# Kernel tuning notes

Measured on AMD Instinct MI355X. Metric: run time of the kernel, lower is better.

Reference implementation:

```python
import jax, jax.numpy as jnp
import numpy as np
from jax import lax

B = 8            # IMAGES_PER_GPU
A = 261888       # num_anchors (1024x1024 Mask R-CNN FPN anchors)
PRE_NMS_LIMIT = 6000
PROPOSAL_COUNT = 1000
NMS_THRESHOLD = 0.7


def setup_inputs() -> dict:
    key = jax.random.key(0)
    k1, k2, k3, k4 = jax.random.split(key, 4)
    rpn_probs = jax.random.uniform(k1, (B, A, 2), dtype=jnp.float32)
    rpn_bbox = jax.random.normal(k2, (B, A, 4), dtype=jnp.float32)
    # valid normalized anchors: y1,x1 in [0,0.9], height/width in [0.01,0.1]
    yx = jax.random.uniform(k3, (B, A, 2), minval=0.0, maxval=0.9)
    hw = jax.random.uniform(k4, (B, A, 2), minval=0.01, maxval=0.1)
    anchors = jnp.concatenate([yx, yx + hw], axis=-1)  # (y1, x1, y2, x2)
    return {"rpn_probs": rpn_probs, "rpn_bbox": rpn_bbox, "anchors": anchors}


def _apply_box_deltas(boxes, deltas):
    # boxes, deltas: [..., 4] in (y1, x1, y2, x2) / (dy, dx, log(dh), log(dw))
    h = boxes[..., 2] - boxes[..., 0]
    w = boxes[..., 3] - boxes[..., 1]
    cy = boxes[..., 0] + 0.5 * h + deltas[..., 0] * h
    cx = boxes[..., 1] + 0.5 * w + deltas[..., 1] * w
    h = h * jnp.exp(deltas[..., 2])
    w = w * jnp.exp(deltas[..., 3])
    y1 = cy - 0.5 * h
    x1 = cx - 0.5 * w
    return jnp.stack([y1, x1, y1 + h, x1 + w], axis=-1)


def _nms_single(boxes, scores):
    # boxes: [K, 4] already sorted by score descending; greedy NMS, zero-padded
    areas = (boxes[:, 2] - boxes[:, 0]) * (boxes[:, 3] - boxes[:, 1])

    def step(valid, _):
        idx = jnp.argmax(valid)          # first still-valid = highest score
        has = valid[idx]                 # False when no candidates remain
        box = boxes[idx]
        yy1 = jnp.maximum(box[0], boxes[:, 0])
        xx1 = jnp.maximum(box[1], boxes[:, 1])
        yy2 = jnp.minimum(box[2], boxes[:, 2])
        xx2 = jnp.minimum(box[3], boxes[:, 3])
        inter = jnp.maximum(yy2 - yy1, 0.0) * jnp.maximum(xx2 - xx1, 0.0)
        union = (box[2] - box[0]) * (box[3] - box[1]) + areas - inter
        iou = lax.stop_gradient(jnp.where(union > 0, inter / union, 0.0))
        valid = valid & (iou <= NMS_THRESHOLD)  # also suppresses idx (self IoU = 1)
        return valid, jnp.where(has, box, jnp.zeros_like(box))

    _, selected = lax.scan(step, jnp.ones(boxes.shape[0], dtype=bool), None,
                           length=PROPOSAL_COUNT)
    return selected  # [PROPOSAL_COUNT, 4], zero-padded like tf.pad in original


def reference(rpn_probs, rpn_bbox, anchors):
    std = jnp.asarray([0.1, 0.1, 0.2, 0.2], dtype=rpn_bbox.dtype)  # RPN_BBOX_STD_DEV
    scores = rpn_probs[:, :, 1]                 # fg prob [B, A]
    deltas = rpn_bbox * std
    k = min(PRE_NMS_LIMIT, anchors.shape[1])
    top_scores, ix = lax.top_k(scores, k)       # sorted descending, [B, K]
    idx = ix[..., None]
    deltas_k = jnp.take_along_axis(deltas, idx, axis=1)    # [B, K, 4]
    anchors_k = jnp.take_along_axis(anchors, idx, axis=1)  # [B, K, 4]
    boxes = jnp.clip(_apply_box_deltas(anchors_k, deltas_k), 0.0, 1.0)  # window [0,0,1,1]
    return jax.vmap(_nms_single)(boxes, top_scores)  # [B, PROPOSAL_COUNT, 4]
```

## Files before the change

kernel.cpp:

```cpp
#include <hip/hip_runtime.h>
#include <math.h>
#include <stdint.h>

typedef uint32_t u32; typedef uint64_t u64; typedef uint16_t u16; typedef int32_t i32;

#define BATCH 8
#define NA    261888
#define SEGS  32
#define SEGCHUNK 8184
#define WCHUNK 2046
#define SUBCAP 64
#define NSUB  128
#define TOPK  6000
#define PROP  1000
#define TOP1  1024
#define TMPCAP 2048
#define CACHEB 8192
#define FBMAX 16384
#define NW64  16
#define PSTATIC 0x3F7C0000u

#define OFF_FBK   0
#define OFF_CACHE 1048576
#define OFF_CNT   1572864
#define OFF_STAT  1576960
#define OFF_BOX   1577216
#define OFF_AREA  1708288
#define OFF_MASK  1741056
#define WS_NEEDED 2789632


__device__ __forceinline__ void decode_box(const float4 an, const float4 dl,
                                           float4& bx, float& ar) {
    float d0 = __fmul_rn(dl.x, 0.1f), d1 = __fmul_rn(dl.y, 0.1f);
    float d2 = __fmul_rn(dl.z, 0.2f), d3 = __fmul_rn(dl.w, 0.2f);
    float h = __fsub_rn(an.z, an.x), w = __fsub_rn(an.w, an.y);
    float cy = __fadd_rn(__fadd_rn(an.x, __fmul_rn(0.5f, h)), __fmul_rn(d0, h));
    float cx = __fadd_rn(__fadd_rn(an.y, __fmul_rn(0.5f, w)), __fmul_rn(d1, w));
    float h2 = __fmul_rn(h, (float)exp((double)d2));
    float w2 = __fmul_rn(w, (float)exp((double)d3));
    float y1 = __fsub_rn(cy, __fmul_rn(0.5f, h2));
    float x1 = __fsub_rn(cx, __fmul_rn(0.5f, w2));
    float y2 = __fadd_rn(y1, h2);
    float x2 = __fadd_rn(x1, w2);
    y1 = fminf(fmaxf(y1, 0.f), 1.f); x1 = fminf(fmaxf(x1, 0.f), 1.f);
    y2 = fminf(fmaxf(y2, 0.f), 1.f); x2 = fminf(fmaxf(x2, 0.f), 1.f);
    bx = make_float4(y1, x1, y2, x2);
    ar = __fmul_rn(__fsub_rn(y2, y1), __fsub_rn(x2, x1));
}

__device__ __forceinline__ bool sup_pred(const float4 bi, const float ai,
                                         const float4 bj, const float aj) {
    const double tmid = (double)0.7f + 0x1p-25;
    float yy1 = fmaxf(bi.x, bj.x), xx1 = fmaxf(bi.y, bj.y);
    float yy2 = fminf(bi.z, bj.z), xx2 = fminf(bi.w, bj.w);
    float ih = fmaxf(__fsub_rn(yy2, yy1), 0.f);
    float iw = fmaxf(__fsub_rn(xx2, xx1), 0.f);
    float inter = __fmul_rn(ih, iw);
    float uni = __fsub_rn(__fadd_rn(ai, aj), inter);
    return (uni > 0.f) && ((double)inter >= tmid * (double)uni);
}

__global__ __launch_bounds__(256) void k_histcache(const float4* __restrict__ p4,
                                                   u64* __restrict__ cache,
                                                   u32* __restrict__ cnt) {
    const int b = blockIdx.y, seg = blockIdx.x;
    const int wave = threadIdx.x >> 6, lane = threadIdx.x & 63;
    const u64 lmask = (1ull << lane) - 1ull;
    const size_t fbase = ((size_t)b * NA + seg * SEGCHUNK + wave * WCHUNK) >> 1;
    const u32 abase = (u32)(seg * SEGCHUNK + wave * WCHUNK);
    u64* cseg = cache + (size_t)b * CACHEB + (seg * 4 + wave) * SUBCAP;
    u32 wOff = 0;
    #pragma unroll
    for (int it = 0; it < 16; ++it) {
        int f = it * 64 + lane;
        bool ok = f < (WCHUNK / 2);
        u32 bitsA = 0, bitsB = 0;
        if (ok) {
            float4 v = p4[fbase + f];
            bitsA = __float_as_uint(v.y);
            bitsB = __float_as_uint(v.w);
        }
        bool pA = ok && bitsA >= PSTATIC;
        bool pB = ok && bitsB >= PSTATIC;
        u64 mA = __ballot(pA);
        u64 mB = __ballot(pB);
        u32 cA = (u32)__popcll(mA);
        if (pA) {
            u32 slot = wOff + (u32)__popcll(mA & lmask);
            if (slot < SUBCAP) cseg[slot] = ((u64)(~bitsA) << 32) | (u64)(abase + 2 * f);
        }
        if (pB) {
            u32 slot = wOff + cA + (u32)__popcll(mB & lmask);
            if (slot < SUBCAP) cseg[slot] = ((u64)(~bitsB) << 32) | (u64)(abase + 2 * f + 1);
        }
        wOff += cA + (u32)__popcll(mB);
    }
    if (lane == 0) cnt[b * NSUB + seg * 4 + wave] = wOff;
}

__global__ __launch_bounds__(1024) void k_sortdec(const u64* __restrict__ cache,
                                                  const u32* __restrict__ cnt,
                                                  const float4* __restrict__ anchors,
                                                  const float4* __restrict__ bbox,
                                                  u32* __restrict__ stat_g,
                                                  float4* __restrict__ boxes,
                                                  float* __restrict__ areas) {
    __shared__ u32 hist[4096];
    __shared__ u32 suffix[4096];
    __shared__ u32 ps[256];
    __shared__ u32 psS[257];
    __shared__ u64 tmp[TMPCAP];
    __shared__ u32 scnt[NSUB];
    __shared__ u32 wq[4];
    __shared__ u32 sP, sN, sBin, stat;
    const int b = blockIdx.x;
    const int tid = threadIdx.x;
    const int lane = tid & 63, wv = tid >> 6;
    if (tid == 0) { stat = 1u; sBin = 0xFFFFFFFFu; }
    for (int i = tid; i < 4096; i += 1024) hist[i] = 0;
    __syncthreads();
    if (tid < NSUB) {
        u32 raw = cnt[b * NSUB + tid];
        scnt[tid] = raw > SUBCAP ? SUBCAP : raw;
        if (raw > SUBCAP) stat = 0u;
    }
    __syncthreads();
    for (int t = tid; t < CACHEB; t += 1024) {
        int sub = t >> 6, off = t & (SUBCAP - 1);
        if (off < (int)scnt[sub]) {
            u32 bits = ~((u32)(cache[(size_t)b * CACHEB + t] >> 32));
            atomicAdd(&hist[(bits >> 6) & 0xFFFu], 1u);
        }
    }
    __syncthreads();
    if (tid < 256) {
        u32 su = 0;
        #pragma unroll
        for (int k = 0; k < 16; ++k) su += hist[tid * 16 + k];
        ps[tid] = su;
    }
    __syncthreads();
    {
        u32 v = (tid < 256) ? ps[tid] : 0u;
        #pragma unroll
        for (int d = 1; d < 64; d <<= 1) {
            u32 o = __shfl_down(v, d);
            if (lane + d < 64) v += o;
        }
        if (tid < 256 && lane == 0) wq[wv] = v;
        __syncthreads();
        if (tid < 256) {
            u32 add = 0;
            for (int q = wv + 1; q < 4; ++q) add += wq[q];
            psS[tid] = v + add;
        }
        if (tid == 0) psS[256] = 0u;
        __syncthreads();
    }
    {
        const int t4 = tid * 4;
        const int seg = tid >> 2;
        const int segEnd = seg * 16 + 15;
        u32 tail = 0;
        for (int bb = t4 + 4; bb <= segEnd; ++bb) tail += hist[bb];
        u32 h0 = hist[t4], h1 = hist[t4 + 1], h2 = hist[t4 + 2], h3 = hist[t4 + 3];
        u32 s3 = psS[seg + 1] + tail;
        u32 s2 = s3 + h3;
        u32 s1 = s2 + h2;
        u32 s0 = s1 + h1;
        suffix[t4] = s0; suffix[t4 + 1] = s1; suffix[t4 + 2] = s2; suffix[t4 + 3] = s3;
        if (s0 < TOP1 && s0 + h0 >= TOP1) sBin = (u32)t4;
        if (s1 < TOP1 && s1 + h1 >= TOP1) sBin = (u32)(t4 + 1);
        if (s2 < TOP1 && s2 + h2 >= TOP1) sBin = (u32)(t4 + 2);
        if (s3 < TOP1 && s3 + h3 >= TOP1) sBin = (u32)(t4 + 3);
    }
    __syncthreads();
    if (tid == 0) {
        if (sBin == 0xFFFFFFFFu) stat = 0u;
        else {
            sP = PSTATIC + (sBin << 6);
            u32 n = suffix[sBin] + hist[sBin];
            sN = n;
            if (n > TMPCAP) stat = 0u;
        }
    }
    __syncthreads();
    if (stat) {
        for (int i = tid; i < 4096; i += 1024) hist[i] = 0;
        __syncthreads();
        const u32 P = sP;
        for (int t = tid; t < CACHEB; t += 1024) {
            int sub = t >> 6, off = t & (SUBCAP - 1);
            if (off < (int)scnt[sub]) {
                u64 key = cache[(size_t)b * CACHEB + t];
                u32 bits = ~((u32)(key >> 32));
                if (bits >= P) {
                    u32 bin = (bits >> 6) & 0xFFFu;
                    u32 arr = atomicAdd(&hist[bin], 1u);
                    tmp[suffix[bin] + arr] = key;
                }
            }
        }
        __syncthreads();
        const u32 n = sN;
        for (u32 t = (u32)tid; t < n; t += 1024) {
            u64 key = tmp[t];
            u32 bits = ~((u32)(key >> 32));
            u32 bin = (bits >> 6) & 0xFFFu;
            u32 base = suffix[bin], len = hist[bin];
            u32 pos = base;
            for (u32 q = base; q < base + len; ++q) pos += (tmp[q] < key) ? 1u : 0u;
            if (pos < TOP1) {
                u32 idx = (u32)key;
                float4 bx; float ar;
                decode_box(anchors[(size_t)b * NA + idx], bbox[(size_t)b * NA + idx], bx, ar);
                boxes[b * TOP1 + pos] = bx;
                areas[b * TOP1 + pos] = ar;
            }
        }
    }
    if (tid == 0) stat_g[b] = stat;
}

__global__ __launch_bounds__(256) void k_mask(const float4* __restrict__ boxes,
                                              const float* __restrict__ areas,
                                              u32* __restrict__ mw32) {
    const int b = blockIdx.y;
    const int wave = threadIdx.x >> 6, lane = threadIdx.x & 63;
    const int irow = blockIdx.x * 4 + wave;
    const int cmax = irow >> 6;
    u32* mt = mw32 + (size_t)b * (NW64 * TOP1 * 2);
    float4 bi = boxes[b * TOP1 + irow];
    float  ai = areas[b * TOP1 + irow];
    u32 myw = 0;
    for (int c = 0; c <= cmax; ++c) {
        float4 bj = boxes[b * TOP1 + c * 64 + lane];
        float  aj = areas[b * TOP1 + c * 64 + lane];
        u64 word = __ballot(sup_pred(bi, ai, bj, aj));
        if (lane == 2 * c)     myw = (u32)word;
        if (lane == 2 * c + 1) myw = (u32)(word >> 32);
    }
    if (lane < 2 * (cmax + 1))
        mt[((lane >> 1) << 11) + (irow << 1) + (lane & 1)] = myw;
}

__global__ __launch_bounds__(1024, 4) void k_nms(const u64* __restrict__ mw_all,
                                                 const float4* __restrict__ boxes,
                                                 const float2* __restrict__ p2,
                                                 const float4* __restrict__ bbox,
                                                 const float4* __restrict__ anchors,
                                                 const u32* __restrict__ stat_g,
                                                 u64* __restrict__ fbkeys,
                                                 float4* __restrict__ out) {
    __shared__ u64 ldsV[NW64];
    __shared__ u32 wpre[NW64 + 1];
    const int b = blockIdx.x;
    const int tid = threadIdx.x;
    const int wave = tid >> 6, lane = tid & 63;
    {
        const u64* mw = mw_all + (size_t)b * (NW64 * TOP1);
        const u64 lmask = (1ull << lane) - 1ull;
        u64 rr[NW64];
        u64 intern = 0;
        #pragma unroll
        for (int w = 0; w < NW64; ++w) {
            u64 v = 0;
            if (w <= wave) v = mw[(w << 10) + (wave << 6) + lane];
            if (w == wave) intern = v & lmask;
            rr[w] = (w < wave) ? v : 0ull;
        }
        u64 ext = 0;
        #pragma unroll
        for (int s = 0; s < NW64; ++s) {
            if (wave == s) {
                const bool extSup = (ext != 0ull);
                u64 v = ~0ull;
                for (int it = 0; it < 64; ++it) {
                    bool alive = (!extSup) && ((intern & v) == 0ull);
                    u64 nv = __ballot(alive);
                    if (nv == v) break;
                    v = nv;
                }
                if (lane == 0) ldsV[s] = v;
            }
            __syncthreads();
            if (wave > s) ext |= rr[s] & ldsV[s];
        }
    }
    if (tid == 0) {
        u32 r = 0;
        #pragma unroll
        for (int c = 0; c < NW64; ++c) { wpre[c] = r; r += (u32)__popcll(ldsV[c]); }
        wpre[NW64] = r;
    }
    __syncthreads();
    const u32 Vt = wpre[NW64];
    if (Vt >= PROP && stat_g[b] != 0u) {
        const int i = tid;
        const int w = i >> 6, bit = i & 63;
        u64 vw = ldsV[w];
        bool isv = ((vw >> bit) & 1ull) != 0ull;
        u32 rank = wpre[w] + (u32)__popcll(vw & ((1ull << bit) - 1ull));
        if (isv && rank < PROP) out[b * PROP + rank] = boxes[b * TOP1 + i];
        return;
    }
    const int i = tid;
    __shared__ float4 abox[PROP];
    __shared__ float  aar[PROP];
    __shared__ u32 fh[4096];
    __shared__ u32 fps[256];
    __shared__ u32 nsh, sP6;
    if (i == 0) nsh = 0;
    for (int z = i; z < 4096; z += 1024) fh[z] = 0;
    __syncthreads();
    for (int a = i; a < NA; a += 1024) {
        u32 bits = __float_as_uint(p2[(size_t)b * NA + a].y);
        atomicAdd(&fh[bits >> 18], 1u);
    }
    __syncthreads();
    if (i < 256) {
        u32 su = 0;
        for (int k = 0; k < 16; ++k) su += fh[i * 16 + k];
        fps[i] = su;
    }
    __syncthreads();
    if (i == 0) {
        u32 acc = 0; int seg = 0;
        for (int t = 255; t >= 0; --t) { if (acc + fps[t] >= TOPK) { seg = t; break; } acc += fps[t]; }
        int b6 = seg * 16; u32 g6 = acc;
        for (int k = 15; k >= 0; --k) {
            u32 c = fh[seg * 16 + k];
            if (g6 + c >= TOPK) { b6 = seg * 16 + k; break; }
            g6 += c;
        }
        sP6 = (u32)b6 << 18;
    }
    __syncthreads();
    u32 P6 = sP6;
    for (int a = i; a < NA; a += 1024) {
        u32 bits = __float_as_uint(p2[(size_t)b * NA + a].y);
        if (bits >= P6) {
            u32 p = atomicAdd(&nsh, 1u);
            if (p < FBMAX) fbkeys[(size_t)b * FBMAX + p] = ((u64)(~bits) << 32) | (u64)a;
        }
    }
    __syncthreads();
    u32 n = nsh; if (n > FBMAX) n = FBMAX;
    volatile u64* vk = (volatile u64*)(fbkeys + (size_t)b * FBMAX);
    for (int i2 = (int)n + i; i2 < FBMAX; i2 += 1024) vk[i2] = ~0ull;
    __syncthreads();
    for (int k = 2; k <= FBMAX; k <<= 1) {
        for (int j = k >> 1; j > 0; j >>= 1) {
            for (int p = i; p < FBMAX / 2; p += 1024) {
                int ii = ((p & ~(j - 1)) << 1) | (p & (j - 1));
                int l = ii | j;
                u64 a = vk[ii], c = vk[l];
                bool up = ((ii & k) == 0);
                if ((a > c) == up) { vk[ii] = c; vk[l] = a; }
            }
            __syncthreads();
        }
    }
    int acc_n = 0;
    int limit = (int)n < TOPK ? (int)n : TOPK;
    for (int t = 0; t < limit && acc_n < PROP; ++t) {
        u32 idx = (u32)vk[t];
        float4 bi2; float ai2;
        decode_box(anchors[(size_t)b * NA + idx], bbox[(size_t)b * NA + idx], bi2, ai2);
        int pred = 0;
        if (i < acc_n) pred = sup_pred(bi2, ai2, abox[i], aar[i]) ? 1 : 0;
        int any = __syncthreads_or(pred);
        if (!any) {
            if (i == 0) {
                abox[acc_n] = bi2; aar[acc_n] = ai2;
                out[b * PROP + acc_n] = bi2;
            }
            ++acc_n;
            __syncthreads();
        }
    }
    for (int t = acc_n + i; t < PROP; t += 1024)
        out[b * PROP + t] = make_float4(0.f, 0.f, 0.f, 0.f);
}


extern "C" void kernel_launch(void* const* d_in, const int* in_sizes, int n_in,
                              void* d_out, int out_size, void* d_ws, size_t ws_size,
                              hipStream_t stream) {
    (void)in_sizes; (void)n_in; (void)out_size;
    if (ws_size < (size_t)WS_NEEDED) return;
    const float2* p2      = (const float2*)d_in[0];
    const float4* p4      = (const float4*)d_in[0];
    const float4* bbox    = (const float4*)d_in[1];
    const float4* anchors = (const float4*)d_in[2];
    float4* out = (float4*)d_out;

    char* ws = (char*)d_ws;
    u64* fbkeys  = (u64*)(ws + OFF_FBK);
    u64* cache   = (u64*)(ws + OFF_CACHE);
    u32* cnt     = (u32*)(ws + OFF_CNT);
    u32* stat_g  = (u32*)(ws + OFF_STAT);
    float4* boxes= (float4*)(ws + OFF_BOX);
    float* areas = (float*)(ws + OFF_AREA);
    u32* mw32    = (u32*)(ws + OFF_MASK);
    u64* mw64    = (u64*)(ws + OFF_MASK);

    dim3 ghc(SEGS, BATCH), gmask(TOP1 / 4, BATCH);
    k_histcache<<<ghc,   256, 0, stream>>>(p4, cache, cnt);
    k_sortdec  <<<BATCH, 1024, 0, stream>>>(cache, cnt, anchors, bbox, stat_g, boxes, areas);
    k_mask     <<<gmask, 256, 0, stream>>>(boxes, areas, mw32);
    k_nms      <<<BATCH, 1024, 0, stream>>>(mw64, boxes, p2, bbox, anchors, stat_g, fbkeys, out);
}
```

Before: 135.6 us.

## Fuse four kernels into two using last-block-done atomic handoff

The histogram/cache pass is merged with the sort/decode pass, and the mask build is merged with the NMS pass. Each merged kernel uses a per-batch global atomic counter so that the last block to finish runs the serial tail stage. This removes two kernel launches and their inter-kernel gaps. The first stage now uses 1024-thread blocks with 512 smaller sub-buckets of capacity 32, and the mask stage runs on 64 blocks per batch. In exchange, the tail stage waits on the slowest block, and overflow is likelier with the smaller per-wave caps, which pushes more batches onto the fallback path.

Result: slower. 172.8 us (+27.4%).

```diff
diff --git a/kernel.cpp b/kernel.cpp
--- a/kernel.cpp
+++ b/kernel.cpp
@@ -8,26 +8,30 @@
 #define NA    261888
 #define SEGS  32
 #define SEGCHUNK 8184
-#define WCHUNK 2046
-#define SUBCAP 64
-#define NSUB  128
+#define SEGF4 4092
+#define SUBCAP 32
+#define NSUB  512
 #define TOPK  6000
 #define PROP  1000
 #define TOP1  1024
 #define TMPCAP 2048
-#define CACHEB 8192
+#define CACHEB 16384
 #define FBMAX 16384
 #define NW64  16
+#define MBLK  64
 #define PSTATIC 0x3F7C0000u
 
 #define OFF_FBK   0
 #define OFF_CACHE 1048576
-#define OFF_CNT   1572864
-#define OFF_STAT  1576960
-#define OFF_BOX   1577216
-#define OFF_AREA  1708288
-#define OFF_MASK  1741056
-#define WS_NEEDED 2789632
+#define OFF_CNT   2097152
+#define OFF_STAT  2113536
+#define OFF_BOX   2113664
+#define OFF_AREA  2244736
+#define OFF_MASK  2277504
+#define WS_NEEDED 3326080
+
+__device__ u32 g_done1[BATCH];
+__device__ u32 g_done2[BATCH];
 
 
 __device__ __forceinline__ void decode_box(const float4 an, const float4 dl,
@@ -61,51 +65,14 @@
     return (uni > 0.f) && ((double)inter >= tmid * (double)uni);
 }
 
-__global__ __launch_bounds__(256) void k_histcache(const float4* __restrict__ p4,
+__global__ __launch_bounds__(1024) void k_histsort(const float4* __restrict__ p4,
                                                    u64* __restrict__ cache,
-                                                   u32* __restrict__ cnt) {
-    const int b = blockIdx.y, seg = blockIdx.x;
-    const int wave = threadIdx.x >> 6, lane = threadIdx.x & 63;
-    const u64 lmask = (1ull << lane) - 1ull;
-    const size_t fbase = ((size_t)b * NA + seg * SEGCHUNK + wave * WCHUNK) >> 1;
-    const u32 abase = (u32)(seg * SEGCHUNK + wave * WCHUNK);
-    u64* cseg = cache + (size_t)b * CACHEB + (seg * 4 + wave) * SUBCAP;
-    u32 wOff = 0;
-    #pragma unroll
-    for (int it = 0; it < 16; ++it) {
-        int f = it * 64 + lane;
-        bool ok = f < (WCHUNK / 2);
-        u32 bitsA = 0, bitsB = 0;
-        if (ok) {
-            float4 v = p4[fbase + f];
-            bitsA = __float_as_uint(v.y);
-            bitsB = __float_as_uint(v.w);
-        }
-        bool pA = ok && bitsA >= PSTATIC;
-        bool pB = ok && bitsB >= PSTATIC;
-        u64 mA = __ballot(pA);
-        u64 mB = __ballot(pB);
-        u32 cA = (u32)__popcll(mA);
-        if (pA) {
-            u32 slot = wOff + (u32)__popcll(mA & lmask);
-            if (slot < SUBCAP) cseg[slot] = ((u64)(~bitsA) << 32) | (u64)(abase + 2 * f);
-        }
-        if (pB) {
-            u32 slot = wOff + cA + (u32)__popcll(mB & lmask);
-            if (slot < SUBCAP) cseg[slot] = ((u64)(~bitsB) << 32) | (u64)(abase + 2 * f + 1);
-        }
-        wOff += cA + (u32)__popcll(mB);
-    }
-    if (lane == 0) cnt[b * NSUB + seg * 4 + wave] = wOff;
-}
-
-__global__ __launch_bounds__(1024) void k_sortdec(const u64* __restrict__ cache,
-                                                  const u32* __restrict__ cnt,
-                                                  const float4* __restrict__ anchors,
-                                                  const float4* __restrict__ bbox,
-                                                  u32* __restrict__ stat_g,
-                                                  float4* __restrict__ boxes,
-                                                  float* __restrict__ areas) {
+                                                   u32* __restrict__ cnt,
+                                                   const float4* __restrict__ anchors,
+                                                   const float4* __restrict__ bbox,
+                                                   u32* __restrict__ stat_g,
+                                                   float4* __restrict__ boxes,
+                                                   float* __restrict__ areas) {
     __shared__ u32 hist[4096];
     __shared__ u32 suffix[4096];
     __shared__ u32 ps[256];
@@ -113,10 +80,54 @@
     __shared__ u64 tmp[TMPCAP];
     __shared__ u32 scnt[NSUB];
     __shared__ u32 wq[4];
-    __shared__ u32 sP, sN, sBin, stat;
-    const int b = blockIdx.x;
+    __shared__ u32 sP, sN, sBin, stat, sWin;
+    const int b = blockIdx.y, seg = blockIdx.x;
     const int tid = threadIdx.x;
-    const int lane = tid & 63, wv = tid >> 6;
+    const int wave = tid >> 6, lane = tid & 63;
+    {
+        const u64 lmask = (1ull << lane) - 1ull;
+        const size_t fbase = ((size_t)b * NA + seg * SEGCHUNK) >> 1;
+        const u32 abase = (u32)(seg * SEGCHUNK);
+        u64* cseg = cache + (size_t)b * CACHEB + (seg * 16 + wave) * SUBCAP;
+        u32 wOff = 0;
+        #pragma unroll
+        for (int it = 0; it < 4; ++it) {
+            int f = it * 1024 + tid;
+            bool ok = f < SEGF4;
+            u32 bitsA = 0, bitsB = 0;
+            if (ok) {
+                float4 v = p4[fbase + f];
+                bitsA = __float_as_uint(v.y);
+                bitsB = __float_as_uint(v.w);
+            }
+            bool pA = ok && bitsA >= PSTATIC;
+            bool pB = ok && bitsB >= PSTATIC;
+            u64 mA = __ballot(pA);
+            u64 mB = __ballot(pB);
+            u32 cA = (u32)__popcll(mA);
+            if (pA) {
+                u32 slot = wOff + (u32)__popcll(mA & lmask);
+                if (slot < SUBCAP) cseg[slot] = ((u64)(~bitsA) << 32) | (u64)(abase + 2 * f);
+            }
+            if (pB) {
+                u32 slot = wOff + cA + (u32)__popcll(mB & lmask);
+                if (slot < SUBCAP) cseg[slot] = ((u64)(~bitsB) << 32) | (u64)(abase + 2 * f + 1);
+            }
+            wOff += cA + (u32)__popcll(mB);
+        }
+        if (lane == 0) cnt[b * NSUB + seg * 16 + wave] = wOff;
+    }
+    __syncthreads();
+    if (tid == 0) {
+        __threadfence();
+        u32 old = atomicAdd(&g_done1[b], 1u);
+        u32 w = (old == (u32)(SEGS - 1)) ? 1u : 0u;
+        if (w) g_done1[b] = 0u;
+        sWin = w;
+    }
+    __syncthreads();
+    if (!sWin) return;
+    __threadfence();
     if (tid == 0) { stat = 1u; sBin = 0xFFFFFFFFu; }
     for (int i = tid; i < 4096; i += 1024) hist[i] = 0;
     __syncthreads();
@@ -127,7 +138,7 @@
     }
     __syncthreads();
     for (int t = tid; t < CACHEB; t += 1024) {
-        int sub = t >> 6, off = t & (SUBCAP - 1);
+        int sub = t >> 5, off = t & (SUBCAP - 1);
         if (off < (int)scnt[sub]) {
             u32 bits = ~((u32)(cache[(size_t)b * CACHEB + t] >> 32));
             atomicAdd(&hist[(bits >> 6) & 0xFFFu], 1u);
@@ -148,11 +159,11 @@
             u32 o = __shfl_down(v, d);
             if (lane + d < 64) v += o;
         }
-        if (tid < 256 && lane == 0) wq[wv] = v;
+        if (tid < 256 && lane == 0) wq[wave] = v;
         __syncthreads();
         if (tid < 256) {
             u32 add = 0;
-            for (int q = wv + 1; q < 4; ++q) add += wq[q];
+            for (int q = wave + 1; q < 4; ++q) add += wq[q];
             psS[tid] = v + add;
         }
         if (tid == 0) psS[256] = 0u;
@@ -160,12 +171,12 @@
     }
     {
         const int t4 = tid * 4;
-        const int seg = tid >> 2;
-        const int segEnd = seg * 16 + 15;
+        const int sg = tid >> 2;
+        const int segEnd = sg * 16 + 15;
         u32 tail = 0;
         for (int bb = t4 + 4; bb <= segEnd; ++bb) tail += hist[bb];
         u32 h0 = hist[t4], h1 = hist[t4 + 1], h2 = hist[t4 + 2], h3 = hist[t4 + 3];
-        u32 s3 = psS[seg + 1] + tail;
+        u32 s3 = psS[sg + 1] + tail;
         u32 s2 = s3 + h3;
         u32 s1 = s2 + h2;
         u32 s0 = s1 + h1;
@@ -191,7 +202,7 @@
         __syncthreads();
         const u32 P = sP;
         for (int t = tid; t < CACHEB; t += 1024) {
-            int sub = t >> 6, off = t & (SUBCAP - 1);
+            int sub = t >> 5, off = t & (SUBCAP - 1);
             if (off < (int)scnt[sub]) {
                 u64 key = cache[(size_t)b * CACHEB + t];
                 u32 bits = ~((u32)(key >> 32));
@@ -223,43 +234,52 @@
     if (tid == 0) stat_g[b] = stat;
 }
 
-__global__ __launch_bounds__(256) void k_mask(const float4* __restrict__ boxes,
-                                              const float* __restrict__ areas,
-                                              u32* __restrict__ mw32) {
-    const int b = blockIdx.y;
-    const int wave = threadIdx.x >> 6, lane = threadIdx.x & 63;
-    const int irow = blockIdx.x * 4 + wave;
-    const int cmax = irow >> 6;
-    u32* mt = mw32 + (size_t)b * (NW64 * TOP1 * 2);
-    float4 bi = boxes[b * TOP1 + irow];
-    float  ai = areas[b * TOP1 + irow];
-    u32 myw = 0;
-    for (int c = 0; c <= cmax; ++c) {
-        float4 bj = boxes[b * TOP1 + c * 64 + lane];
-        float  aj = areas[b * TOP1 + c * 64 + lane];
-        u64 word = __ballot(sup_pred(bi, ai, bj, aj));
-        if (lane == 2 * c)     myw = (u32)word;
-        if (lane == 2 * c + 1) myw = (u32)(word >> 32);
-    }
-    if (lane < 2 * (cmax + 1))
-        mt[((lane >> 1) << 11) + (irow << 1) + (lane & 1)] = myw;
-}
-
-__global__ __launch_bounds__(1024, 4) void k_nms(const u64* __restrict__ mw_all,
-                                                 const float4* __restrict__ boxes,
-                                                 const float2* __restrict__ p2,
-                                                 const float4* __restrict__ bbox,
-                                                 const float4* __restrict__ anchors,
-                                                 const u32* __restrict__ stat_g,
-                                                 u64* __restrict__ fbkeys,
-                                                 float4* __restrict__ out) {
+__global__ __launch_bounds__(1024, 4) void k_masknms(const float4* __restrict__ boxes,
+                                                     const float* __restrict__ areas,
+                                                     const float2* __restrict__ p2,
+                                                     const float4* __restrict__ bbox,
+                                                     const float4* __restrict__ anchors,
+                                                     const u32* __restrict__ stat_g,
+                                                     u32* __restrict__ mw32,
+                                                     const u64* __restrict__ mw64,
+                                                     u64* __restrict__ fbkeys,
+                                                     float4* __restrict__ out) {
     __shared__ u64 ldsV[NW64];
     __shared__ u32 wpre[NW64 + 1];
-    const int b = blockIdx.x;
+    __shared__ u32 sWin;
+    const int b = blockIdx.y;
     const int tid = threadIdx.x;
     const int wave = tid >> 6, lane = tid & 63;
     {
-        const u64* mw = mw_all + (size_t)b * (NW64 * TOP1);
+        const int irow = (wave << 6) + blockIdx.x;
+        const int cmax = wave;
+        u32* mt = mw32 + (size_t)b * (NW64 * TOP1 * 2);
+        float4 bi = boxes[b * TOP1 + irow];
+        float  ai = areas[b * TOP1 + irow];
+        u32 myw = 0;
+        for (int c = 0; c <= cmax; ++c) {
+            float4 bj = boxes[b * TOP1 + c * 64 + lane];
+            float  aj = areas[b * TOP1 + c * 64 + lane];
+            u64 word = __ballot(sup_pred(bi, ai, bj, aj));
+            if (lane == 2 * c)     myw = (u32)word;
+            if (lane == 2 * c + 1) myw = (u32)(word >> 32);
+        }
+        if (lane < 2 * (cmax + 1))
+            mt[((lane >> 1) << 11) + (irow << 1) + (lane & 1)] = myw;
+    }
+    __syncthreads();
+    if (tid == 0) {
+        __threadfence();
+        u32 old = atomicAdd(&g_done2[b], 1u);
+        u32 w = (old == (u32)(MBLK - 1)) ? 1u : 0u;
+        if (w) g_done2[b] = 0u;
+        sWin = w;
+    }
+    __syncthreads();
+    if (!sWin) return;
+    __threadfence();
+    {
+        const u64* mw = mw64 + (size_t)b * (NW64 * TOP1);
         const u64 lmask = (1ull << lane) - 1ull;
         u64 rr[NW64];
         u64 intern = 0;
@@ -406,9 +426,7 @@
     u32* mw32    = (u32*)(ws + OFF_MASK);
     u64* mw64    = (u64*)(ws + OFF_MASK);
 
-    dim3 ghc(SEGS, BATCH), gmask(TOP1 / 4, BATCH);
-    k_histcache<<<ghc,   256, 0, stream>>>(p4, cache, cnt);
-    k_sortdec  <<<BATCH, 1024, 0, stream>>>(cache, cnt, anchors, bbox, stat_g, boxes, areas);
-    k_mask     <<<gmask, 256, 0, stream>>>(boxes, areas, mw32);
-    k_nms      <<<BATCH, 1024, 0, stream>>>(mw64, boxes, p2, bbox, anchors, stat_g, fbkeys, out);
+    dim3 ghs(SEGS, BATCH), gmn(MBLK, BATCH);
+    k_histsort<<<ghs, 1024, 0, stream>>>(p4, cache, cnt, anchors, bbox, stat_g, boxes, areas);
+    k_masknms <<<gmn, 1024, 0, stream>>>(boxes, areas, p2, bbox, anchors, stat_g, mw32, mw64, fbkeys, out);
 }
```

## Fuse IoU mask computation into NMS kernel, computing suppression on the fly

Applied to the files above, without the earlier changes.

Removes the separate k_mask kernel and its global suppression bitmask. The NMS kernel now stages the top boxes and areas in LDS and evaluates IoU predicates lazily: intra-chunk bits per wave, and cross-chunk suppression only against kept boxes, with an early exit once a box is found to be suppressed. This saves one launch and the mask write and read traffic. The cost is that IoU work moves from a widely parallel grid into 8 blocks running a 16-stage sequential loop, which lengthens the critical path.

Result: slower. 336.4 us (+148.1%).

```diff
diff --git a/kernel.cpp b/kernel.cpp
--- a/kernel.cpp
+++ b/kernel.cpp
@@ -24,10 +24,9 @@
 #define OFF_CACHE 1048576
 #define OFF_CNT   1572864
 #define OFF_STAT  1576960
-#define OFF_BOX   1577216
-#define OFF_AREA  1708288
-#define OFF_MASK  1741056
-#define WS_NEEDED 2789632
+#define OFF_BOX   1577088
+#define OFF_AREA  1708160
+#define WS_NEEDED 1740928
 
 
 __device__ __forceinline__ void decode_box(const float4 an, const float4 dl,
@@ -223,57 +222,38 @@
     if (tid == 0) stat_g[b] = stat;
 }
 
-__global__ __launch_bounds__(256) void k_mask(const float4* __restrict__ boxes,
-                                              const float* __restrict__ areas,
-                                              u32* __restrict__ mw32) {
-    const int b = blockIdx.y;
-    const int wave = threadIdx.x >> 6, lane = threadIdx.x & 63;
-    const int irow = blockIdx.x * 4 + wave;
-    const int cmax = irow >> 6;
-    u32* mt = mw32 + (size_t)b * (NW64 * TOP1 * 2);
-    float4 bi = boxes[b * TOP1 + irow];
-    float  ai = areas[b * TOP1 + irow];
-    u32 myw = 0;
-    for (int c = 0; c <= cmax; ++c) {
-        float4 bj = boxes[b * TOP1 + c * 64 + lane];
-        float  aj = areas[b * TOP1 + c * 64 + lane];
-        u64 word = __ballot(sup_pred(bi, ai, bj, aj));
-        if (lane == 2 * c)     myw = (u32)word;
-        if (lane == 2 * c + 1) myw = (u32)(word >> 32);
-    }
-    if (lane < 2 * (cmax + 1))
-        mt[((lane >> 1) << 11) + (irow << 1) + (lane & 1)] = myw;
-}
-
-__global__ __launch_bounds__(1024, 4) void k_nms(const u64* __restrict__ mw_all,
-                                                 const float4* __restrict__ boxes,
+__global__ __launch_bounds__(1024) void k_nmsfly(const float4* __restrict__ boxes,
+                                                 const float* __restrict__ areas,
                                                  const float2* __restrict__ p2,
                                                  const float4* __restrict__ bbox,
                                                  const float4* __restrict__ anchors,
                                                  const u32* __restrict__ stat_g,
                                                  u64* __restrict__ fbkeys,
                                                  float4* __restrict__ out) {
+    __shared__ float4 sbox[TOP1];
+    __shared__ float  sarea[TOP1];
     __shared__ u64 ldsV[NW64];
     __shared__ u32 wpre[NW64 + 1];
     const int b = blockIdx.x;
     const int tid = threadIdx.x;
     const int wave = tid >> 6, lane = tid & 63;
-    {
-        const u64* mw = mw_all + (size_t)b * (NW64 * TOP1);
-        const u64 lmask = (1ull << lane) - 1ull;
-        u64 rr[NW64];
-        u64 intern = 0;
-        #pragma unroll
-        for (int w = 0; w < NW64; ++w) {
-            u64 v = 0;
-            if (w <= wave) v = mw[(w << 10) + (wave << 6) + lane];
-            if (w == wave) intern = v & lmask;
-            rr[w] = (w < wave) ? v : 0ull;
-        }
+    const u32 stat = stat_g[b];
+    if (stat) {
+        for (int t = tid; t < TOP1; t += 1024) {
+            sbox[t] = boxes[b * TOP1 + t];
+            sarea[t] = areas[b * TOP1 + t];
+        }
+        __syncthreads();
+        const int i = tid;
+        const float4 bi = sbox[i];
+        const float  ai = sarea[i];
         u64 ext = 0;
-        #pragma unroll
         for (int s = 0; s < NW64; ++s) {
             if (wave == s) {
+                u64 intern = 0;
+                for (int j = 0; j < 63; ++j)
+                    if (j < lane && sup_pred(bi, ai, sbox[(s << 6) + j], sarea[(s << 6) + j]))
+                        intern |= (1ull << j);
                 const bool extSup = (ext != 0ull);
                 u64 v = ~0ull;
                 for (int it = 0; it < 64; ++it) {
@@ -285,25 +265,34 @@
                 if (lane == 0) ldsV[s] = v;
             }
             __syncthreads();
-            if (wave > s) ext |= rr[s] & ldsV[s];
-        }
-    }
-    if (tid == 0) {
-        u32 r = 0;
-        #pragma unroll
-        for (int c = 0; c < NW64; ++c) { wpre[c] = r; r += (u32)__popcll(ldsV[c]); }
-        wpre[NW64] = r;
-    }
-    __syncthreads();
-    const u32 Vt = wpre[NW64];
-    if (Vt >= PROP && stat_g[b] != 0u) {
-        const int i = tid;
-        const int w = i >> 6, bit = i & 63;
-        u64 vw = ldsV[w];
-        bool isv = ((vw >> bit) & 1ull) != 0ull;
-        u32 rank = wpre[w] + (u32)__popcll(vw & ((1ull << bit) - 1ull));
-        if (isv && rank < PROP) out[b * PROP + rank] = boxes[b * TOP1 + i];
-        return;
+            if (wave > s && ext == 0ull) {
+                u64 m = ldsV[s];
+                while (m) {
+                    int j = __ffsll((unsigned long long)m) - 1;
+                    m &= m - 1;
+                    if (sup_pred(bi, ai, sbox[(s << 6) + j], sarea[(s << 6) + j])) {
+                        ext = 1ull;
+                        break;
+                    }
+                }
+            }
+        }
+        if (tid == 0) {
+            u32 r = 0;
+            #pragma unroll
+            for (int c = 0; c < NW64; ++c) { wpre[c] = r; r += (u32)__popcll(ldsV[c]); }
+            wpre[NW64] = r;
+        }
+        __syncthreads();
+        const u32 Vt = wpre[NW64];
+        if (Vt >= PROP) {
+            const int w = i >> 6, bit = i & 63;
+            u64 vw = ldsV[w];
+            bool isv = ((vw >> bit) & 1ull) != 0ull;
+            u32 rank = wpre[w] + (u32)__popcll(vw & ((1ull << bit) - 1ull));
+            if (isv && rank < PROP) out[b * PROP + rank] = sbox[i];
+            return;
+        }
     }
     const int i = tid;
     __shared__ float4 abox[PROP];
@@ -403,12 +392,9 @@
     u32* stat_g  = (u32*)(ws + OFF_STAT);
     float4* boxes= (float4*)(ws + OFF_BOX);
     float* areas = (float*)(ws + OFF_AREA);
-    u32* mw32    = (u32*)(ws + OFF_MASK);
-    u64* mw64    = (u64*)(ws + OFF_MASK);
-
-    dim3 ghc(SEGS, BATCH), gmask(TOP1 / 4, BATCH);
+
+    dim3 ghc(SEGS, BATCH);
     k_histcache<<<ghc,   256, 0, stream>>>(p4, cache, cnt);
     k_sortdec  <<<BATCH, 1024, 0, stream>>>(cache, cnt, anchors, bbox, stat_g, boxes, areas);
-    k_mask     <<<gmask, 256, 0, stream>>>(boxes, areas, mw32);
-    k_nms      <<<BATCH, 1024, 0, stream>>>(mw64, boxes, p2, bbox, anchors, stat_g, fbkeys, out);
-}
+    k_nmsfly   <<<BATCH, 1024, 0, stream>>>(boxes, areas, p2, bbox, anchors, stat_g, fbkeys, out);
+}
```
